# Kernel tuning notes

Hardware: AMD Instinct MI355X
Metric: run time of the kernel (lower is better)

## Reference

```python
import jax, jax.numpy as jnp
import numpy as np

D, FF, E, K = 1024, 1024, 8, 2  # d_model, ffn_dim, n_experts, top_k
B, S = 4, 1024


def _gelu(x):
    # torch F.gelu default is the exact erf form
    return jax.nn.gelu(x, approximate=False)


def setup_inputs() -> dict:
    key = jax.random.key(0)
    ks = jax.random.split(key, 12)
    s = 0.02
    return {
        "x": jax.random.normal(ks[0], (B, S, D), jnp.float32),
        "gate_w": jax.random.normal(ks[1], (D, E), jnp.float32) * s,
        "gate_b": jnp.zeros((E,), jnp.float32),
        # shared expert (n_shared = 1)
        "sw1": jax.random.normal(ks[2], (D, FF), jnp.float32) * s,
        "sb1": jnp.zeros((FF,), jnp.float32),
        "sw2": jax.random.normal(ks[3], (FF, D), jnp.float32) * s,
        "sb2": jnp.zeros((D,), jnp.float32),
        # routed experts, stacked over E
        "w1": jax.random.normal(ks[4], (E, D, FF), jnp.float32) * s,
        "b1": jnp.zeros((E, FF), jnp.float32),
        "w2": jax.random.normal(ks[5], (E, FF, D), jnp.float32) * s,
        "b2": jnp.zeros((E, D), jnp.float32),
    }


def reference(x, gate_w, gate_b, sw1, sb1, sw2, sb2, w1, b1, w2, b2):
    Bb, Ss, Dm = x.shape
    t = x.reshape(-1, Dm)  # [T, D]
    T = t.shape[0]

    # shared expert(s)
    shared = _gelu(t @ sw1 + sb1) @ sw2 + sb2  # [T, D]

    # gating: softmax over experts, then top-k
    probs = jax.nn.softmax(t @ gate_w + gate_b, axis=-1)  # [T, E]
    topk_p, topk_i = jax.lax.top_k(probs, K)  # [T, K]

    # combine weights: sparse [T, E] with top-k probs (top_k indices are distinct)
    combine = jnp.zeros((T, E), t.dtype).at[
        jnp.arange(T)[:, None], topk_i
    ].set(topk_p)

    # expert FFNs computed densely, combined with sparse routing weights;
    # mathematically identical to the masked gather-GEMM-scatter loop
    h = _gelu(jnp.einsum("td,edf->etf", t, w1) + b1[:, None, :])  # [E, T, FF]
    y = jnp.einsum("etf,efd->etd", h, w2) + b2[:, None, :]        # [E, T, D]
    routed = jnp.einsum("te,etd->td", combine, y)                  # [T, D]

    return (routed + shared).reshape(Bb, Ss, Dm)
```

## Files before the change

kernel.cpp:

```cpp
#include <hip/hip_runtime.h>
#include <hip/hip_bf16.h>


typedef short short8 __attribute__((ext_vector_type(8)));
typedef float f32x4  __attribute__((ext_vector_type(4)));

#define T_TOK 4096
#define NSLOT 8192

#define OFF_XB    (size_t)0
#define OFF_W1T   (size_t)8388608
#define OFF_W2T   (size_t)25165824
#define OFF_SW1T  (size_t)41943040
#define OFF_SW2T  (size_t)44040192
#define OFF_HS    (size_t)46137344
#define OFF_HR    (size_t)54525952
#define OFF_META  (size_t)73400320
#define OFF_ROWMAP (size_t)73400576
#define OFF_ROWW  (size_t)73437440
#define OFF_TKI   (size_t)73474304
#define OFF_TKP   (size_t)73507072

__device__ __forceinline__ unsigned short f2bf(float f) {
  __hip_bfloat16 h = __float2bfloat16(f);
  return __builtin_bit_cast(unsigned short, h);
}
__device__ __forceinline__ float gelu_exact(float x) {
  return 0.5f * x * (1.0f + erff(x * 0.70710678118654752f));
}

#define GLOAD16(g, l)                                                          \
  __builtin_amdgcn_global_load_lds(                                            \
      (const __attribute__((address_space(1))) void*)(g),                      \
      (__attribute__((address_space(3))) void*)(l), 16, 0, 0)


__global__ void k_transpose(const float* __restrict__ w1, const float* __restrict__ w2,
                            const float* __restrict__ sw1, const float* __restrict__ sw2,
                            unsigned short* __restrict__ w1t, unsigned short* __restrict__ w2t,
                            unsigned short* __restrict__ sw1t, unsigned short* __restrict__ sw2t) {
  __shared__ float tile[32][33];
  int z = blockIdx.z;
  const float* src; unsigned short* dst;
  if (z < 8)       { src = w1 + (size_t)z * 1048576;        dst = w1t + (size_t)z * 1048576; }
  else if (z < 16) { src = w2 + (size_t)(z - 8) * 1048576;  dst = w2t + (size_t)(z - 8) * 1048576; }
  else if (z == 16){ src = sw1; dst = sw1t; }
  else             { src = sw2; dst = sw2t; }
  int tx = threadIdx.x, ty = threadIdx.y;
  int gx = blockIdx.x * 32 + tx;
#pragma unroll
  for (int j = 0; j < 4; j++) {
    int gy = blockIdx.y * 32 + ty + j * 8;
    tile[ty + j * 8][tx] = src[(size_t)gy * 1024 + gx];
  }
  __syncthreads();
#pragma unroll
  for (int j = 0; j < 4; j++) {
    int orow = blockIdx.x * 32 + ty + j * 8;
    int ocol = blockIdx.y * 32 + tx;
    dst[(size_t)orow * 1024 + ocol] = f2bf(tile[tx][ty + j * 8]);
  }
}

__global__ void k_convert_x(const float* __restrict__ x, unsigned short* __restrict__ xb) {
  int i = blockIdx.x * blockDim.x + threadIdx.x;
  float4 v = ((const float4*)x)[i];
  ushort4 o;
  o.x = f2bf(v.x); o.y = f2bf(v.y); o.z = f2bf(v.z); o.w = f2bf(v.w);
  ((ushort4*)xb)[i] = o;
}

__global__ void k_gate(const float* __restrict__ x, const float* __restrict__ gw,
                       const float* __restrict__ gb, int* __restrict__ tki,
                       float* __restrict__ tkp) {
  int wv = threadIdx.x >> 6, l = threadIdx.x & 63;
  int t = blockIdx.x * 4 + wv;
  float acc[8] = {0, 0, 0, 0, 0, 0, 0, 0};
  const float* xr = x + (size_t)t * 1024;
#pragma unroll
  for (int j = 0; j < 16; j++) {
    int k = j * 64 + l;
    float xv = xr[k];
    const float4* g4 = (const float4*)(gw + (size_t)k * 8);
    float4 ga = g4[0], gbv = g4[1];
    acc[0] += xv * ga.x; acc[1] += xv * ga.y; acc[2] += xv * ga.z; acc[3] += xv * ga.w;
    acc[4] += xv * gbv.x; acc[5] += xv * gbv.y; acc[6] += xv * gbv.z; acc[7] += xv * gbv.w;
  }
#pragma unroll
  for (int off = 32; off > 0; off >>= 1) {
#pragma unroll
    for (int e = 0; e < 8; e++) acc[e] += __shfl_xor(acc[e], off);
  }
  if (l == 0) {
    float lg[8], p[8];
    float m = -1e30f;
#pragma unroll
    for (int e = 0; e < 8; e++) { lg[e] = acc[e] + gb[e]; m = fmaxf(m, lg[e]); }
    float s = 0.f;
#pragma unroll
    for (int e = 0; e < 8; e++) { p[e] = expf(lg[e] - m); s += p[e]; }
    float inv = 1.0f / s;
#pragma unroll
    for (int e = 0; e < 8; e++) p[e] *= inv;
    int i0 = 0;
#pragma unroll
    for (int e = 1; e < 8; e++) if (p[e] > p[i0]) i0 = e;
    int i1 = (i0 == 0) ? 1 : 0;
#pragma unroll
    for (int e = 0; e < 8; e++) if (e != i0 && p[e] > p[i1]) i1 = e;
    tki[t * 2] = i0; tki[t * 2 + 1] = i1;
    tkp[t * 2] = p[i0]; tkp[t * 2 + 1] = p[i1];
  }
}

__global__ void k_count(const int* __restrict__ tki, int* __restrict__ counts) {
  int e = blockIdx.x, tid = threadIdx.x;
  int c = 0;
  for (int i = tid; i < NSLOT; i += 256) c += (tki[i] == e);
  __shared__ int red[256];
  red[tid] = c;
  __syncthreads();
#pragma unroll
  for (int s = 128; s > 0; s >>= 1) {
    if (tid < s) red[tid] += red[tid + s];
    __syncthreads();
  }
  if (tid == 0) counts[e] = red[0];
}

__global__ void k_plan(const int* __restrict__ counts, int* __restrict__ base) {
  int off = 0;
  for (int e = 0; e < 8; e++) {
    base[e] = off;
    off += (counts[e] + 63) & ~63;
  }
}

__global__ void k_scatter(const int* __restrict__ tki, const float* __restrict__ tkp,
                          const int* __restrict__ base, int* __restrict__ rowmap,
                          float* __restrict__ roww) {
  int e = blockIdx.x, tid = threadIdx.x;
  int lane = tid & 63, wv = tid >> 6;
  __shared__ int warpsum[4];
  __shared__ int blockoff;
  if (tid == 0) blockoff = base[e];
  __syncthreads();
  for (int i0 = 0; i0 < NSLOT; i0 += 256) {
    int i = i0 + tid;
    bool pred = (tki[i] == e);
    unsigned long long mask = __ballot(pred);
    int wpre = __popcll(mask & ((1ull << lane) - 1));
    if (lane == 0) warpsum[wv] = __popcll(mask);
    __syncthreads();
    int wbase = 0;
    for (int w = 0; w < wv; w++) wbase += warpsum[w];
    int total = warpsum[0] + warpsum[1] + warpsum[2] + warpsum[3];
    int boff = blockoff;
    if (pred) {
      int pos = boff + wbase + wpre;
      rowmap[pos] = i >> 1;
      roww[pos] = tkp[i];
    }
    __syncthreads();
    if (tid == 0) blockoff = boff + total;
    __syncthreads();
  }
}

template <int PHASE>
__global__ __launch_bounds__(256, 4) void k_ffn(
    const unsigned short* __restrict__ As,
    const unsigned short* __restrict__ Ar,
    const unsigned short* __restrict__ Bsh, const float* __restrict__ bsh,
    const unsigned short* __restrict__ Brt, const float* __restrict__ brt,
    unsigned short* __restrict__ Hsh, unsigned short* __restrict__ Hrt,
    float* __restrict__ outf,
    const int* __restrict__ rowmap, const float* __restrict__ roww,
    const int* __restrict__ counts, const int* __restrict__ bases) {
  __shared__ unsigned short ldsA[64 * 64];
  __shared__ unsigned short ldsB[128 * 64];

  int z = blockIdx.z;
  int row0 = blockIdx.y * 64;
  int nrows, rbase = 0;
  const unsigned short* Bmat;
  const float* bvec;
  const unsigned short* Amat;
  if (z == 0) {
    nrows = T_TOK;
    Bmat = Bsh; bvec = bsh; Amat = As;
  } else {
    int e = z - 1;
    nrows = counts[e]; rbase = bases[e];
    if (row0 >= nrows) return;
    Bmat = Brt + (size_t)e * 1048576;
    bvec = brt + (size_t)e * 1024;
    Amat = (PHASE == 1) ? As : Ar;
  }
  int n0 = blockIdx.x * 128;
  int tid = threadIdx.x, wave = tid >> 6, lane = tid & 63;
  int wm = wave >> 1, wn = wave & 1;

  long arow[2];
#pragma unroll
  for (int i = 0; i < 2; i++) {
    int q = i * 4 + wave;
    int m = (q * 64 + lane) >> 3;
    int r = row0 + m;
    if (r >= nrows) r = nrows - 1;
    if (z == 0)            arow[i] = r;
    else if (PHASE == 1)   arow[i] = rowmap[rbase + r];
    else                   arow[i] = rbase + r;
  }

  f32x4 acc[2][4];
#pragma unroll
  for (int i = 0; i < 2; i++)
#pragma unroll
    for (int j = 0; j < 4; j++) acc[i][j] = (f32x4){0.f, 0.f, 0.f, 0.f};

  for (int k0 = 0; k0 < 1024; k0 += 64) {
#pragma unroll
    for (int i = 0; i < 2; i++) {
      int q = i * 4 + wave;
      int c = q * 64 + lane;
      int m = c >> 3, s = c & 7;
      int ks = s ^ (m & 7);
      GLOAD16(Amat + arow[i] * 1024 + k0 + ks * 8, &ldsA[q * 512]);
    }
#pragma unroll
    for (int i = 0; i < 4; i++) {
      int q = i * 4 + wave;
      int c = q * 64 + lane;
      int n = c >> 3, s = c & 7;
      int ks = s ^ (n & 7);
      GLOAD16(Bmat + (size_t)(n0 + n) * 1024 + k0 + ks * 8, &ldsB[q * 512]);
    }
    __syncthreads();
#pragma unroll
    for (int kk = 0; kk < 2; kk++) {
      short8 af[2], bfr[4];
      int kc0 = kk * 4 + (lane >> 4);
#pragma unroll
      for (int fi = 0; fi < 2; fi++) {
        int m = wm * 32 + fi * 16 + (lane & 15);
        int slot = kc0 ^ (m & 7);
        af[fi] = *(const short8*)&ldsA[m * 64 + slot * 8];
      }
#pragma unroll
      for (int fj = 0; fj < 4; fj++) {
        int n = wn * 64 + fj * 16 + (lane & 15);
        int slot = kc0 ^ (n & 7);
        bfr[fj] = *(const short8*)&ldsB[n * 64 + slot * 8];
      }
#pragma unroll
      for (int fi = 0; fi < 2; fi++)
#pragma unroll
        for (int fj = 0; fj < 4; fj++)
          acc[fi][fj] = __builtin_amdgcn_mfma_f32_16x16x32_bf16(af[fi], bfr[fj], acc[fi][fj], 0, 0, 0);
    }
    __syncthreads();
  }

#pragma unroll
  for (int fi = 0; fi < 2; fi++) {
#pragma unroll
    for (int rg = 0; rg < 4; rg++) {
      int lr = wm * 32 + fi * 16 + (lane >> 4) * 4 + rg;
      int r = row0 + lr;
      if (r >= nrows) continue;
      if (PHASE == 1) {
        unsigned short* dst = (z == 0) ? (Hsh + (size_t)r * 1024)
                                       : (Hrt + (size_t)(rbase + r) * 1024);
#pragma unroll
        for (int fj = 0; fj < 4; fj++) {
          int col = n0 + wn * 64 + fj * 16 + (lane & 15);
          dst[col] = f2bf(gelu_exact(acc[fi][fj][rg] + bvec[col]));
        }
      } else {
        if (z == 0) {
#pragma unroll
          for (int fj = 0; fj < 4; fj++) {
            int col = n0 + wn * 64 + fj * 16 + (lane & 15);
            atomicAdd(&outf[(size_t)r * 1024 + col], acc[fi][fj][rg] + bvec[col]);
          }
        } else {
          int tok = rowmap[rbase + r];
          float p = roww[rbase + r];
#pragma unroll
          for (int fj = 0; fj < 4; fj++) {
            int col = n0 + wn * 64 + fj * 16 + (lane & 15);
            atomicAdd(&outf[(size_t)tok * 1024 + col], p * (acc[fi][fj][rg] + bvec[col]));
          }
        }
      }
    }
  }
}

extern "C" void kernel_launch(void* const* d_in, const int* in_sizes, int n_in,
                              void* d_out, int out_size, void* d_ws, size_t ws_size,
                              hipStream_t stream) {
  const float* x   = (const float*)d_in[0];
  const float* gw  = (const float*)d_in[1];
  const float* gb  = (const float*)d_in[2];
  const float* sw1 = (const float*)d_in[3];
  const float* sb1 = (const float*)d_in[4];
  const float* sw2 = (const float*)d_in[5];
  const float* sb2 = (const float*)d_in[6];
  const float* w1  = (const float*)d_in[7];
  const float* b1  = (const float*)d_in[8];
  const float* w2  = (const float*)d_in[9];
  const float* b2  = (const float*)d_in[10];
  float* out = (float*)d_out;
  char* ws = (char*)d_ws;

  unsigned short* xb   = (unsigned short*)(ws + OFF_XB);
  unsigned short* w1t  = (unsigned short*)(ws + OFF_W1T);
  unsigned short* w2t  = (unsigned short*)(ws + OFF_W2T);
  unsigned short* sw1t = (unsigned short*)(ws + OFF_SW1T);
  unsigned short* sw2t = (unsigned short*)(ws + OFF_SW2T);
  unsigned short* Hs   = (unsigned short*)(ws + OFF_HS);
  unsigned short* Hr   = (unsigned short*)(ws + OFF_HR);
  int*   counts = (int*)(ws + OFF_META);
  int*   basev  = counts + 8;
  int*   rowmap = (int*)(ws + OFF_ROWMAP);
  float* roww   = (float*)(ws + OFF_ROWW);
  int*   tki    = (int*)(ws + OFF_TKI);
  float* tkp    = (float*)(ws + OFF_TKP);

  k_transpose<<<dim3(32, 32, 18), dim3(32, 8), 0, stream>>>(w1, w2, sw1, sw2, w1t, w2t, sw1t, sw2t);
  k_convert_x<<<4096, 256, 0, stream>>>(x, xb);
  k_gate<<<1024, 256, 0, stream>>>(x, gw, gb, tki, tkp);
  k_count<<<8, 256, 0, stream>>>(tki, counts);
  k_plan<<<1, 1, 0, stream>>>(counts, basev);
  k_scatter<<<8, 256, 0, stream>>>(tki, tkp, basev, rowmap, roww);
  hipMemsetAsync(out, 0, (size_t)out_size * sizeof(float), stream);

  k_ffn<1><<<dim3(8, 64, 9), 256, 0, stream>>>(xb, xb, sw1t, sb1, w1t, b1, Hs, Hr,
                                               nullptr, rowmap, roww, counts, basev);
  k_ffn<2><<<dim3(8, 64, 9), 256, 0, stream>>>(Hs, Hr, sw2t, sb2, w2t, b2, nullptr, nullptr,
                                               out, rowmap, roww, counts, basev);
}
```

Before: 192.2 us.

## Enlarge FFN GEMM row tile to 128 and fuse routing kernels into one

Doubles the M tile of the FFN GEMM from 64 to 128 rows, so each wave computes a 64x64 output block with 16 accumulators and each B-tile load is reused across twice as many rows. Expert padding is raised to 128 to match. It also merges the count, plan and scatter kernels into a single routing kernel that counts all experts in every block, which removes two launches and one serialized single-thread kernel. The grid still launches 64 row-blocks, so half of them now exit early. Accumulators and LDS usage double, which may lower occupancy, and padding waste per expert grows.

```diff
diff --git a/kernel.cpp b/kernel.cpp
--- a/kernel.cpp
+++ b/kernel.cpp
@@ -113,38 +113,43 @@
   }
 }
 
-__global__ void k_count(const int* __restrict__ tki, int* __restrict__ counts) {
-  int e = blockIdx.x, tid = threadIdx.x;
-  int c = 0;
-  for (int i = tid; i < NSLOT; i += 256) c += (tki[i] == e);
-  __shared__ int red[256];
-  red[tid] = c;
-  __syncthreads();
-#pragma unroll
-  for (int s = 128; s > 0; s >>= 1) {
-    if (tid < s) red[tid] += red[tid + s];
-    __syncthreads();
-  }
-  if (tid == 0) counts[e] = red[0];
-}
-
-__global__ void k_plan(const int* __restrict__ counts, int* __restrict__ base) {
-  int off = 0;
-  for (int e = 0; e < 8; e++) {
-    base[e] = off;
-    off += (counts[e] + 63) & ~63;
-  }
-}
-
-__global__ void k_scatter(const int* __restrict__ tki, const float* __restrict__ tkp,
-                          const int* __restrict__ base, int* __restrict__ rowmap,
-                          float* __restrict__ roww) {
+__global__ void k_route(const int* __restrict__ tki, const float* __restrict__ tkp,
+                        int* __restrict__ counts, int* __restrict__ basev,
+                        int* __restrict__ rowmap, float* __restrict__ roww) {
   int e = blockIdx.x, tid = threadIdx.x;
   int lane = tid & 63, wv = tid >> 6;
+  int c[8] = {0, 0, 0, 0, 0, 0, 0, 0};
+  for (int i = tid; i < NSLOT; i += 256) {
+    int v = tki[i];
+#pragma unroll
+    for (int q = 0; q < 8; q++) c[q] += (v == q);
+  }
+  __shared__ int red[8][64];
+#pragma unroll
+  for (int q = 0; q < 8; q++) {
+#pragma unroll
+    for (int off = 32; off > 0; off >>= 1) c[q] += __shfl_xor(c[q], off);
+  }
+  if (lane == 0) {
+#pragma unroll
+    for (int q = 0; q < 8; q++) red[q][wv] = c[q];
+  }
+  __syncthreads();
+  __shared__ int cnt_s[8], base_s[8];
+  if (tid == 0) {
+    int off = 0;
+#pragma unroll
+    for (int q = 0; q < 8; q++) {
+      int cq = red[q][0] + red[q][1] + red[q][2] + red[q][3];
+      cnt_s[q] = cq; base_s[q] = off;
+      off += (cq + 127) & ~127;
+    }
+    counts[e] = cnt_s[e];
+    basev[e] = base_s[e];
+  }
+  __syncthreads();
   __shared__ int warpsum[4];
-  __shared__ int blockoff;
-  if (tid == 0) blockoff = base[e];
-  __syncthreads();
+  int wpos = base_s[e];
   for (int i0 = 0; i0 < NSLOT; i0 += 256) {
     int i = i0 + tid;
     bool pred = (tki[i] == e);
@@ -155,14 +160,12 @@
     int wbase = 0;
     for (int w = 0; w < wv; w++) wbase += warpsum[w];
     int total = warpsum[0] + warpsum[1] + warpsum[2] + warpsum[3];
-    int boff = blockoff;
     if (pred) {
-      int pos = boff + wbase + wpre;
+      int pos = wpos + wbase + wpre;
       rowmap[pos] = i >> 1;
       roww[pos] = tkp[i];
     }
-    __syncthreads();
-    if (tid == 0) blockoff = boff + total;
+    wpos += total;
     __syncthreads();
   }
 }
@@ -177,17 +180,18 @@
     float* __restrict__ outf,
     const int* __restrict__ rowmap, const float* __restrict__ roww,
     const int* __restrict__ counts, const int* __restrict__ bases) {
-  __shared__ unsigned short ldsA[64 * 64];
+  __shared__ unsigned short ldsA[128 * 64];
   __shared__ unsigned short ldsB[128 * 64];
 
   int z = blockIdx.z;
-  int row0 = blockIdx.y * 64;
+  int row0 = blockIdx.y * 128;
   int nrows, rbase = 0;
   const unsigned short* Bmat;
   const float* bvec;
   const unsigned short* Amat;
   if (z == 0) {
     nrows = T_TOK;
+    if (row0 >= nrows) return;
     Bmat = Bsh; bvec = bsh; Amat = As;
   } else {
     int e = z - 1;
@@ -201,9 +205,9 @@
   int tid = threadIdx.x, wave = tid >> 6, lane = tid & 63;
   int wm = wave >> 1, wn = wave & 1;
 
-  long arow[2];
-#pragma unroll
-  for (int i = 0; i < 2; i++) {
+  long arow[4];
+#pragma unroll
+  for (int i = 0; i < 4; i++) {
     int q = i * 4 + wave;
     int m = (q * 64 + lane) >> 3;
     int r = row0 + m;
@@ -213,15 +217,15 @@
     else                   arow[i] = rbase + r;
   }
 
-  f32x4 acc[2][4];
-#pragma unroll
-  for (int i = 0; i < 2; i++)
+  f32x4 acc[4][4];
+#pragma unroll
+  for (int i = 0; i < 4; i++)
 #pragma unroll
     for (int j = 0; j < 4; j++) acc[i][j] = (f32x4){0.f, 0.f, 0.f, 0.f};
 
   for (int k0 = 0; k0 < 1024; k0 += 64) {
 #pragma unroll
-    for (int i = 0; i < 2; i++) {
+    for (int i = 0; i < 4; i++) {
       int q = i * 4 + wave;
       int c = q * 64 + lane;
       int m = c >> 3, s = c & 7;
@@ -239,11 +243,11 @@
     __syncthreads();
 #pragma unroll
     for (int kk = 0; kk < 2; kk++) {
-      short8 af[2], bfr[4];
+      short8 af[4], bfr[4];
       int kc0 = kk * 4 + (lane >> 4);
 #pragma unroll
-      for (int fi = 0; fi < 2; fi++) {
-        int m = wm * 32 + fi * 16 + (lane & 15);
+      for (int fi = 0; fi < 4; fi++) {
+        int m = wm * 64 + fi * 16 + (lane & 15);
         int slot = kc0 ^ (m & 7);
         af[fi] = *(const short8*)&ldsA[m * 64 + slot * 8];
       }
@@ -254,7 +258,7 @@
         bfr[fj] = *(const short8*)&ldsB[n * 64 + slot * 8];
       }
 #pragma unroll
-      for (int fi = 0; fi < 2; fi++)
+      for (int fi = 0; fi < 4; fi++)
 #pragma unroll
         for (int fj = 0; fj < 4; fj++)
           acc[fi][fj] = __builtin_amdgcn_mfma_f32_16x16x32_bf16(af[fi], bfr[fj], acc[fi][fj], 0, 0, 0);
@@ -263,10 +267,10 @@
   }
 
 #pragma unroll
-  for (int fi = 0; fi < 2; fi++) {
+  for (int fi = 0; fi < 4; fi++) {
 #pragma unroll
     for (int rg = 0; rg < 4; rg++) {
-      int lr = wm * 32 + fi * 16 + (lane >> 4) * 4 + rg;
+      int lr = wm * 64 + fi * 16 + (lane >> 4) * 4 + rg;
       int r = row0 + lr;
       if (r >= nrows) continue;
       if (PHASE == 1) {
@@ -329,13 +333,11 @@
   int*   tki    = (int*)(ws + OFF_TKI);
   float* tkp    = (float*)(ws + OFF_TKP);
 
+  hipMemsetAsync(out, 0, (size_t)out_size * sizeof(float), stream);
   k_transpose<<<dim3(32, 32, 18), dim3(32, 8), 0, stream>>>(w1, w2, sw1, sw2, w1t, w2t, sw1t, sw2t);
   k_convert_x<<<4096, 256, 0, stream>>>(x, xb);
   k_gate<<<1024, 256, 0, stream>>>(x, gw, gb, tki, tkp);
-  k_count<<<8, 256, 0, stream>>>(tki, counts);
-  k_plan<<<1, 1, 0, stream>>>(counts, basev);
-  k_scatter<<<8, 256, 0, stream>>>(tki, tkp, basev, rowmap, roww);
-  hipMemsetAsync(out, 0, (size_t)out_size * sizeof(float), stream);
+  k_route<<<8, 256, 0, stream>>>(tki, tkp, counts, basev, rowmap, roww);
 
   k_ffn<1><<<dim3(8, 64, 9), 256, 0, stream>>>(xb, xb, sw1t, sb1, w1t, b1, Hs, Hr,
                                                nullptr, rowmap, roww, counts, basev);
```

After: 192.8 us. About the same (+0.3%).
